# Performance work log

Hardware: AMD Instinct MI355X
Metric: run time of the kernel (lower is better)

The kernel has to match this reference:

```python
import jax, jax.numpy as jnp
import numpy as np

B, S, DM, H, DF = 2, 2048, 1024, 16, 4096
HD = DM // H
EPS = 1e-6
NEG = -1e9


def setup_inputs() -> dict:
    key = jax.random.key(0)
    ks = jax.random.split(key, 16)
    sc = 1.0 / np.sqrt(DM)
    scf = 1.0 / np.sqrt(DF)
    return {
        "x": jax.random.normal(ks[0], (B, S, DM), jnp.float32),
        "src_mask": jax.random.randint(ks[1], (B, 1, 1, S), 0, 2, jnp.int32),
        "Wq": jax.random.normal(ks[2], (DM, DM), jnp.float32) * sc,
        "bq": jnp.zeros((DM,), jnp.float32),
        "Wk": jax.random.normal(ks[3], (DM, DM), jnp.float32) * sc,
        "bk": jnp.zeros((DM,), jnp.float32),
        "Wv": jax.random.normal(ks[4], (DM, DM), jnp.float32) * sc,
        "bv": jnp.zeros((DM,), jnp.float32),
        "Wo": jax.random.normal(ks[5], (DM, DM), jnp.float32) * sc,
        "bo": jnp.zeros((DM,), jnp.float32),
        "W1": jax.random.normal(ks[6], (DM, DF), jnp.float32) * sc,
        "b1": jnp.zeros((DF,), jnp.float32),
        "W2": jax.random.normal(ks[7], (DF, DM), jnp.float32) * scf,
        "b2": jnp.zeros((DM,), jnp.float32),
        "alpha1": jnp.ones((1,), jnp.float32),
        "beta1": jnp.ones((1,), jnp.float32),
        "alpha2": jnp.ones((1,), jnp.float32),
        "beta2": jnp.ones((1,), jnp.float32),
    }


def layer_norm(x, alpha, beta):
    # torch: mean + unbiased std (ddof=1), scalar alpha/beta, eps added to std
    mean = jnp.mean(x, axis=-1, keepdims=True)
    std = jnp.std(x, axis=-1, keepdims=True, ddof=1)
    return alpha * (x - mean) / (std + EPS) + beta


def mha(x, mask, Wq, bq, Wk, bk, Wv, bv, Wo, bo):
    def split(t):  # [B,S,DM] -> [B,H,S,HD]
        return t.reshape(B, S, H, HD).transpose(0, 2, 1, 3)
    q = split(x @ Wq + bq)
    k = split(x @ Wk + bk)
    v = split(x @ Wv + bv)
    scores = jnp.einsum("bhqd,bhkd->bhqk", q, k) / np.sqrt(HD)
    scores = jnp.where(mask == 0, NEG, scores)
    probs = jax.nn.softmax(scores, axis=-1)  # dropout in eval mode = identity
    out = jnp.einsum("bhqk,bhkd->bhqd", probs, v)
    out = out.transpose(0, 2, 1, 3).reshape(B, S, DM)
    return out @ Wo + bo


def reference(x, src_mask, Wq, bq, Wk, bk, Wv, bv, Wo, bo, W1, b1, W2, b2,
              alpha1, beta1, alpha2, beta2):
    # pre-norm residual: x + attn(norm(x)); dropout disabled (eval)
    n1 = layer_norm(x, alpha1, beta1)
    h = x + mha(n1, src_mask, Wq, bq, Wk, bk, Wv, bv, Wo, bo)
    n2 = layer_norm(h, alpha2, beta2)
    ff = jax.nn.relu(n2 @ W1 + b1) @ W2 + b2
    return h + ff
```

## Files before the change

kernel.cpp:

```cpp
#include <hip/hip_runtime.h>
#include <hip/hip_bf16.h>

#define SEQ   2048
#define BATCH 2
#define DMODEL 1024
#define DFF   4096
#define NHEAD 16
#define HDIM  64
#define NTOK  (BATCH*SEQ)

typedef short s8v __attribute__((ext_vector_type(8)));
typedef float f4v __attribute__((ext_vector_type(4)));

__device__ __forceinline__ float b2f(unsigned short u) {
    union { unsigned int i; float f; } v; v.i = ((unsigned int)u) << 16; return v.f;
}
__device__ __forceinline__ unsigned short f2b(float f) {
    union { unsigned int i; float f; } v; v.f = f;
    unsigned int r = v.i + 0x7FFFu + ((v.i >> 16) & 1u);
    return (unsigned short)(r >> 16);
}
__device__ __forceinline__ ushort2 cvt_pk(float a, float b) {
    __hip_bfloat162 h = __float22bfloat162_rn(float2{ a, b });
    return *(ushort2*)&h;
}

__device__ __forceinline__ f4v mfma_bf16(s8v a, s8v b, f4v c) {
    return __builtin_amdgcn_mfma_f32_16x16x32_bf16(a, b, c, 0, 0, 0);
}

__device__ __forceinline__ void gload_lds16(const void* g, void* l) {
    __builtin_amdgcn_global_load_lds(
        (const __attribute__((address_space(1))) unsigned int*)g,
        (__attribute__((address_space(3))) unsigned int*)l, 16, 0, 0);
}

template<int N> __device__ __forceinline__ void wait_vmcnt() {
    if constexpr (N == 8)      asm volatile("s_waitcnt vmcnt(8)" ::: "memory");
    else if constexpr (N == 6) asm volatile("s_waitcnt vmcnt(6)" ::: "memory");
    else if constexpr (N == 4) asm volatile("s_waitcnt vmcnt(4)" ::: "memory");
    else if constexpr (N == 2) asm volatile("s_waitcnt vmcnt(2)" ::: "memory");
    else                       asm volatile("s_waitcnt vmcnt(0)" ::: "memory");
}

__device__ __forceinline__ void tp_tile(const float* __restrict__ src,
                                        unsigned short* __restrict__ dst,
                                        int R, int C, int br, int bc, int t,
                                        unsigned short* tl) {
    for (int i = 0; i < 16; i++) {
        int idx = t + 256 * i;
        int r = idx >> 6, c = idx & 63;
        tl[r * 65 + c] = f2b(src[(size_t)(br * 64 + r) * C + bc * 64 + c]);
    }
    __syncthreads();
    for (int i = 0; i < 16; i++) {
        int idx = t + 256 * i;
        int r2 = idx >> 6, c2 = idx & 63;
        dst[(size_t)(bc * 64 + r2) * R + br * 64 + c2] = tl[c2 * 65 + r2];
    }
}

__global__ __launch_bounds__(256) void prep_weights(const float* __restrict__ Wq,
                                                    const float* __restrict__ Wk,
                                                    const float* __restrict__ Wv,
                                                    const float* __restrict__ Wo,
                                                    const float* __restrict__ W1,
                                                    const float* __restrict__ W2,
                                                    const float* __restrict__ bq,
                                                    const float* __restrict__ bk,
                                                    const float* __restrict__ bv,
                                                    const float* __restrict__ x,
                                                    const float* __restrict__ a1,
                                                    const float* __restrict__ be1,
                                                    unsigned short* __restrict__ Wqkv_t,
                                                    unsigned short* __restrict__ Wo_t,
                                                    unsigned short* __restrict__ W1_t,
                                                    unsigned short* __restrict__ W2_t,
                                                    float* __restrict__ bqkv,
                                                    unsigned short* __restrict__ n1) {
    __shared__ unsigned short tl[64 * 65];
    __shared__ float red[8];
    const int t = threadIdx.x;
    const int bx = blockIdx.x, by = blockIdx.y, z = blockIdx.z;
    if (z < 4) {
        const float* src = (z == 0) ? Wq : (z == 1) ? Wk : (z == 2) ? Wv : Wo;
        unsigned short* dst = (z == 3) ? Wo_t : Wqkv_t + (size_t)z * 1024 * 1024;
        tp_tile(src, dst, 1024, 1024, bx, by, t, tl);
    } else if (z == 4) {
        for (int i = 0; i < 4; i++) {
            tp_tile(W1, W1_t, 1024, 4096, bx, by + 16 * i, t, tl);
            __syncthreads();
        }
    } else if (z == 5) {
        if (bx == 0 && by == 0) {
            for (int i = 0; i < 12; i++) {
                int idx = t + 256 * i;
                if (idx < 1024) bqkv[idx] = bq[idx];
                else if (idx < 2048) bqkv[idx] = bk[idx - 1024];
                else if (idx < 3072) bqkv[idx] = bv[idx - 2048];
            }
        }
        for (int i = 0; i < 4; i++) {
            tp_tile(W2, W2_t, 4096, 1024, bx + 16 * i, by, t, tl);
            __syncthreads();
        }
    } else {
        const int row = (z - 6) * 256 + by * 16 + bx;
        const float* xr = x + (size_t)row * DMODEL;
        float4 u = ((const float4*)xr)[t];
        float v[4] = { u.x, u.y, u.z, u.w };
        float s = v[0] + v[1] + v[2] + v[3];
        float sq = v[0]*v[0] + v[1]*v[1] + v[2]*v[2] + v[3]*v[3];
        for (int off = 32; off; off >>= 1) { s += __shfl_xor(s, off); sq += __shfl_xor(sq, off); }
        int wave = t >> 6, lane = t & 63;
        if (!lane) { red[wave] = s; red[4 + wave] = sq; }
        __syncthreads();
        s = red[0] + red[1] + red[2] + red[3];
        sq = red[4] + red[5] + red[6] + red[7];
        float mean = s * (1.f / DMODEL);
        float var = (sq - (float)DMODEL * mean * mean) * (1.f / (DMODEL - 1));
        var = var < 0.f ? 0.f : var;
        float inv = a1[0] / (sqrtf(var) + 1e-6f);
        float bt = be1[0];
        uint2 ou;
        unsigned short r0 = f2b((v[0] - mean) * inv + bt);
        unsigned short r1 = f2b((v[1] - mean) * inv + bt);
        unsigned short r2 = f2b((v[2] - mean) * inv + bt);
        unsigned short r3 = f2b((v[3] - mean) * inv + bt);
        ou.x = (unsigned int)r0 | ((unsigned int)r1 << 16);
        ou.y = (unsigned int)r2 | ((unsigned int)r3 << 16);
        ((uint2*)(n1 + (size_t)row * DMODEL))[t] = ou;
    }
}

__global__ __launch_bounds__(256) void mask_scan(const int* __restrict__ msk,
                                                 int* __restrict__ idx,
                                                 float* __restrict__ maskc2,
                                                 int* __restrict__ ntiles) {
    const int b = blockIdx.x, t = threadIdx.x;
    const int base = b * SEQ;
    __shared__ int wsum[4];
    int k[8]; int cnt = 0;
    for (int j = 0; j < 8; j++) {
        k[j] = (msk[base + t * 8 + j] != 0) ? 1 : 0;
        cnt += k[j];
    }
    const int lane = t & 63, wv = t >> 6;
    int pre = cnt;
    for (int off = 1; off < 64; off <<= 1) {
        int n = __shfl_up(pre, off);
        if (lane >= off) pre += n;
    }
    if (lane == 63) wsum[wv] = pre;
    __syncthreads();
    const int Nb = wsum[0] + wsum[1] + wsum[2] + wsum[3];
    int woff = 0;
    for (int w = 0; w < wv; w++) woff += wsum[w];
    const int excl = woff + pre - cnt;
    for (int j = 0; j < 8; j++) {
        int g = t * 8 + j;
        idx[base + g] = 0;
        maskc2[base + g] = (g < Nb) ? 0.f : -1e9f;
    }
    __syncthreads();
    int pos = excl;
    for (int j = 0; j < 8; j++) {
        if (k[j]) { idx[base + pos] = t * 8 + j; pos++; }
    }
    if (t == 0) ntiles[b] = (Nb + 63) >> 6;
}

__global__ __launch_bounds__(256) void pack_kv(const unsigned short* __restrict__ Kb,
                                               const unsigned short* __restrict__ Vb,
                                               const int* __restrict__ idx,
                                               const int* __restrict__ ntiles,
                                               unsigned short* __restrict__ Kc,
                                               unsigned short* __restrict__ Vc) {
    __shared__ unsigned short tl[64 * 65];
    const int t = threadIdx.x;
    const int kt = blockIdx.x, h = blockIdx.y, b = blockIdx.z;
    if (kt >= ntiles[b]) return;
    const int* idxb = idx + b * SEQ + kt * 64;
    const unsigned short* srcK = Kb + (size_t)b * SEQ * 1024 + h * HDIM;
    unsigned short* dstK = Kc + ((size_t)((b * NHEAD + h) * 32 + kt)) * 4096;
    for (int i = 0; i < 2; i++) {
        int ci = t + 256 * i;
        int r = ci >> 3, cp = ci & 7;
        int cl = cp ^ (r & 7);
        int row = idxb[r];
        *(uint4*)&dstK[ci * 8] = *(const uint4*)&srcK[(size_t)row * 1024 + cl * 8];
    }
    const unsigned short* srcV = Vb + (size_t)b * SEQ * 1024 + h * HDIM;
    for (int i = 0; i < 16; i++) {
        int idx2 = t + 256 * i;
        int r = idx2 >> 6, c = idx2 & 63;
        int row = idxb[r];
        tl[r * 65 + c] = srcV[(size_t)row * 1024 + c];
    }
    __syncthreads();
    unsigned short* dstV = Vc + ((size_t)((b * NHEAD + h) * 32 + kt)) * 4096;
    for (int i = 0; i < 2; i++) {
        int ci = t + 256 * i;
        int r = ci >> 3, cp = ci & 7;
        int cl = cp ^ (r & 7);
        ushort4 e0, e1;
        e0.x = tl[(cl * 8 + 0) * 65 + r]; e0.y = tl[(cl * 8 + 1) * 65 + r];
        e0.z = tl[(cl * 8 + 2) * 65 + r]; e0.w = tl[(cl * 8 + 3) * 65 + r];
        e1.x = tl[(cl * 8 + 4) * 65 + r]; e1.y = tl[(cl * 8 + 5) * 65 + r];
        e1.z = tl[(cl * 8 + 6) * 65 + r]; e1.w = tl[(cl * 8 + 7) * 65 + r];
        *(ushort4*)&dstV[ci * 8]     = e0;
        *(ushort4*)&dstV[ci * 8 + 4] = e1;
    }
}

__global__ __launch_bounds__(256) void ln_kernel(const float* __restrict__ x,
                                                 const float* __restrict__ al,
                                                 const float* __restrict__ be,
                                                 unsigned short* __restrict__ o) {
    const int row = blockIdx.x;
    const float* xr = x + (size_t)row * DMODEL;
    float4 u = ((const float4*)xr)[threadIdx.x];
    float v[4] = { u.x, u.y, u.z, u.w };
    float s = v[0] + v[1] + v[2] + v[3];
    float sq = v[0]*v[0] + v[1]*v[1] + v[2]*v[2] + v[3]*v[3];
    for (int off = 32; off; off >>= 1) { s += __shfl_xor(s, off); sq += __shfl_xor(sq, off); }
    __shared__ float red[8];
    int wave = threadIdx.x >> 6, lane = threadIdx.x & 63;
    if (!lane) { red[wave] = s; red[4 + wave] = sq; }
    __syncthreads();
    s = red[0] + red[1] + red[2] + red[3];
    sq = red[4] + red[5] + red[6] + red[7];
    float mean = s * (1.f / DMODEL);
    float var = (sq - (float)DMODEL * mean * mean) * (1.f / (DMODEL - 1));
    var = var < 0.f ? 0.f : var;
    float inv = al[0] / (sqrtf(var) + 1e-6f);
    float bt = be[0];
    uint2 ou;
    unsigned short r0 = f2b((v[0] - mean) * inv + bt);
    unsigned short r1 = f2b((v[1] - mean) * inv + bt);
    unsigned short r2 = f2b((v[2] - mean) * inv + bt);
    unsigned short r3 = f2b((v[3] - mean) * inv + bt);
    ou.x = (unsigned int)r0 | ((unsigned int)r1 << 16);
    ou.y = (unsigned int)r2 | ((unsigned int)r3 << 16);
    ((uint2*)(o + (size_t)row * DMODEL))[threadIdx.x] = ou;
}


template<int SPAN, int NL>
__device__ __forceinline__ void stage_half(const unsigned short* __restrict__ mat,
                                           int base, int K, int k0, int q,
                                           unsigned short* sdst, int t) {
#pragma unroll
    for (int i = 0; i < NL; i++) {
        int ci = i * 512 + t;
        int rl = ci >> 3;
        int c  = (ci & 7) ^ (rl & 7);
        int gr = (rl / SPAN) * (2 * SPAN) + q * SPAN + (rl % SPAN);
        gload_lds16(mat + (size_t)(base + gr) * K + k0 + c * 8, sdst + (size_t)ci * 8);
    }
}

__device__ __forceinline__ const s8v* afrag(const unsigned short* sA, int mi, int s,
                                            int wm, int l16, int quad) {
    int q = mi >> 2;
    int rl = wm * 64 + (mi & 3) * 16 + l16;
    return (const s8v*)&sA[q * 8192 + rl * 64 + (((s * 4 + quad) ^ (l16 & 7)) * 8)];
}
template<int BN>
__device__ __forceinline__ const s8v* bfrag(const unsigned short* sB, int ni, int s,
                                            int wn, int l16, int quad) {
    constexpr int NQB = BN / 128;
    int q = ni / NQB;
    int rl = wn * (BN / 8) + (ni % NQB) * 16 + l16;
    return (const s8v*)&sB[q * (BN * 32) + rl * 64 + (((s * 4 + quad) ^ (l16 & 7)) * 8)];
}

template<int BN>
__device__ __forceinline__ void half_8ph(const unsigned short* __restrict__ A,
                                         const unsigned short* __restrict__ Bt,
                                         int m0, int n0, int K, int kT1, int kT2, bool doT2,
                                         const unsigned short* sAr, const unsigned short* sBr,
                                         unsigned short* sA_this, unsigned short* sB_this,
                                         unsigned short* sA_oth,
                                         int wm, int wn, int l16, int quad, int t,
                                         f4v acc[8][BN / 64]) {
    constexpr int NFC = BN / 64, NQB = NFC / 2;
    constexpr int BSPAN = BN / 8, BNL = BN / 128, BHALF = BN * 32;
    s8v a[4][2], b[NFC][2];
#pragma unroll
    for (int m2 = 0; m2 < 4; m2++) {
        a[m2][0] = *afrag(sAr, m2, 0, wm, l16, quad);
        a[m2][1] = *afrag(sAr, m2, 1, wm, l16, quad);
    }
#pragma unroll
    for (int nb = 0; nb < NQB; nb++) {
        b[nb][0] = *bfrag<BN>(sBr, nb, 0, wn, l16, quad);
        b[nb][1] = *bfrag<BN>(sBr, nb, 1, wn, l16, quad);
    }
    stage_half<64, 2>(A, m0, K, kT1, 1, sA_oth + 8192, t);
    __builtin_amdgcn_s_barrier();
    asm volatile("s_waitcnt lgkmcnt(0)" ::: "memory");
    __builtin_amdgcn_s_setprio(1);
#pragma unroll
    for (int m2 = 0; m2 < 4; m2++)
#pragma unroll
        for (int nb = 0; nb < NQB; nb++) {
            acc[m2][nb] = mfma_bf16(a[m2][0], b[nb][0], acc[m2][nb]);
            acc[m2][nb] = mfma_bf16(a[m2][1], b[nb][1], acc[m2][nb]);
        }
    __builtin_amdgcn_s_setprio(0);
    __builtin_amdgcn_s_barrier();
#pragma unroll
    for (int nb = 0; nb < NQB; nb++) {
        b[NQB + nb][0] = *bfrag<BN>(sBr, NQB + nb, 0, wn, l16, quad);
        b[NQB + nb][1] = *bfrag<BN>(sBr, NQB + nb, 1, wn, l16, quad);
    }
    if (doT2) stage_half<64, 2>(A, m0, K, kT2, 0, sA_this, t);
    __builtin_amdgcn_s_barrier();
    asm volatile("s_waitcnt lgkmcnt(0)" ::: "memory");
    __builtin_amdgcn_s_setprio(1);
#pragma unroll
    for (int m2 = 0; m2 < 4; m2++)
#pragma unroll
        for (int nb = 0; nb < NQB; nb++) {
            acc[m2][NQB + nb] = mfma_bf16(a[m2][0], b[NQB + nb][0], acc[m2][NQB + nb]);
            acc[m2][NQB + nb] = mfma_bf16(a[m2][1], b[NQB + nb][1], acc[m2][NQB + nb]);
        }
    __builtin_amdgcn_s_setprio(0);
    __builtin_amdgcn_s_barrier();
#pragma unroll
    for (int m2 = 0; m2 < 4; m2++) {
        a[m2][0] = *afrag(sAr, 4 + m2, 0, wm, l16, quad);
        a[m2][1] = *afrag(sAr, 4 + m2, 1, wm, l16, quad);
    }
    if (doT2) stage_half<BSPAN, BNL>(Bt, n0, K, kT2, 0, sB_this, t);
    __builtin_amdgcn_s_barrier();
    asm volatile("s_waitcnt lgkmcnt(0)" ::: "memory");
    __builtin_amdgcn_s_setprio(1);
#pragma unroll
    for (int m2 = 0; m2 < 4; m2++)
#pragma unroll
        for (int nb = 0; nb < NQB; nb++) {
            acc[4 + m2][nb] = mfma_bf16(a[m2][0], b[nb][0], acc[4 + m2][nb]);
            acc[4 + m2][nb] = mfma_bf16(a[m2][1], b[nb][1], acc[4 + m2][nb]);
        }
    __builtin_amdgcn_s_setprio(0);
    __builtin_amdgcn_s_barrier();
    if (doT2) {
        stage_half<BSPAN, BNL>(Bt, n0, K, kT2, 1, sB_this + BHALF, t);
        if constexpr (BN == 256) wait_vmcnt<6>(); else wait_vmcnt<4>();
    } else {
        wait_vmcnt<0>();
    }
    __builtin_amdgcn_s_barrier();
    __builtin_amdgcn_s_setprio(1);
#pragma unroll
    for (int m2 = 0; m2 < 4; m2++)
#pragma unroll
        for (int nb = 0; nb < NQB; nb++) {
            acc[4 + m2][NQB + nb] = mfma_bf16(a[m2][0], b[NQB + nb][0], acc[4 + m2][NQB + nb]);
            acc[4 + m2][NQB + nb] = mfma_bf16(a[m2][1], b[NQB + nb][1], acc[4 + m2][NQB + nb]);
        }
    __builtin_amdgcn_s_setprio(0);
    __builtin_amdgcn_s_barrier();
}

template<int BN>
__device__ __forceinline__ void comp_full(const unsigned short* sA, const unsigned short* sB,
                                          int wm, int wn, int l16, int quad,
                                          f4v acc[8][BN / 64]) {
    constexpr int NFC = BN / 64;
    s8v b[NFC][2];
#pragma unroll
    for (int ni = 0; ni < NFC; ni++) {
        b[ni][0] = *bfrag<BN>(sB, ni, 0, wn, l16, quad);
        b[ni][1] = *bfrag<BN>(sB, ni, 1, wn, l16, quad);
    }
#pragma unroll
    for (int mi = 0; mi < 8; mi++) {
        s8v a0 = *afrag(sA, mi, 0, wm, l16, quad);
        s8v a1 = *afrag(sA, mi, 1, wm, l16, quad);
#pragma unroll
        for (int ni = 0; ni < NFC; ni++) {
            acc[mi][ni] = mfma_bf16(a0, b[ni][0], acc[mi][ni]);
            acc[mi][ni] = mfma_bf16(a1, b[ni][1], acc[mi][ni]);
        }
    }
}

template<bool RELU, bool RES, typename CT, bool SPLIT3, int BN>
__global__ __launch_bounds__(512, 2) void gemm256(const unsigned short* __restrict__ A,
                                                  const unsigned short* __restrict__ Bt,
                                                  const float* __restrict__ bias,
                                                  const float* __restrict__ res,
                                                  CT* __restrict__ C,
                                                  float* __restrict__ pbuf,
                                                  int M, int N, int K, int KS) {
    constexpr int NFC = BN / 64;
    constexpr int BHALF = BN * 32;
    __shared__ __align__(16) unsigned short smA[2][256 * 64];
    __shared__ __align__(16) unsigned short smB[2][BN * 64];
    const int t = threadIdx.x;
    const int wave = t >> 6, lane = t & 63;
    const int quad = lane >> 4, l16 = lane & 15;
    const int wm = wave >> 2, wn = wave & 3;
    const int m0 = blockIdx.x * 256, n0 = blockIdx.y * BN;
    const int z = blockIdx.z;
    const int kbeg = z * KS;
    const int nt = KS >> 6;

    f4v acc[8][NFC] = {};

    stage_half<64, 2>(A, m0, K, kbeg, 0, smA[0], t);
    stage_half<64, 2>(A, m0, K, kbeg, 1, smA[0] + 8192, t);
    stage_half<BN / 8, BN / 128>(Bt, n0, K, kbeg, 0, smB[0], t);
    stage_half<BN / 8, BN / 128>(Bt, n0, K, kbeg, 1, smB[0] + BHALF, t);
    stage_half<64, 2>(A, m0, K, kbeg + 64, 0, smA[1], t);
    stage_half<BN / 8, BN / 128>(Bt, n0, K, kbeg + 64, 0, smB[1], t);
    stage_half<BN / 8, BN / 128>(Bt, n0, K, kbeg + 64, 1, smB[1] + BHALF, t);
    if constexpr (BN == 256) wait_vmcnt<6>(); else wait_vmcnt<4>();
    __builtin_amdgcn_s_barrier();

    for (int i = 0; i < nt / 2 - 1; ++i) {
        const int kb = kbeg + 2 * i * 64;
        half_8ph<BN>(A, Bt, m0, n0, K, kb + 64, kb + 128, true,
                     smA[0], smB[0], smA[0], smB[0], smA[1],
                     wm, wn, l16, quad, t, acc);
        half_8ph<BN>(A, Bt, m0, n0, K, kb + 128, kb + 192, true,
                     smA[1], smB[1], smA[1], smB[1], smA[0],
                     wm, wn, l16, quad, t, acc);
    }
    half_8ph<BN>(A, Bt, m0, n0, K, kbeg + (nt - 1) * 64, 0, false,
                 smA[0], smB[0], smA[0], smB[0], smA[1],
                 wm, wn, l16, quad, t, acc);
    __builtin_amdgcn_s_setprio(1);
    comp_full<BN>(smA[1], smB[1], wm, wn, l16, quad, acc);
    __builtin_amdgcn_s_setprio(0);

#pragma unroll
    for (int mi = 0; mi < 8; mi++) {
#pragma unroll
        for (int ni = 0; ni < NFC; ni++) {
            const int col = n0 + wn * (NFC * 16) + ni * 16 + l16;
            const int row0 = m0 + wm * 128 + mi * 16 + quad * 4;
            if (z == 0) {
                const float bv = bias[col];
#pragma unroll
                for (int r = 0; r < 4; r++) {
                    float v = acc[mi][ni][r] + bv;
                    if (RELU) v = v > 0.f ? v : 0.f;
                    if (RES) v += res[(size_t)(row0 + r) * N + col];
                    size_t cidx;
                    if constexpr (SPLIT3)
                        cidx = (size_t)(col >> 10) * ((size_t)NTOK * 1024)
                             + (size_t)(row0 + r) * 1024 + (col & 1023);
                    else
                        cidx = (size_t)(row0 + r) * N + col;
                    if constexpr (sizeof(CT) == 2)
                        C[cidx] = f2b(v);
                    else
                        C[cidx] = v;
                }
            } else {
#pragma unroll
                for (int r = 0; r < 4; r++)
                    pbuf[(size_t)(z - 1) * M * N + (size_t)(row0 + r) * N + col]
                        = acc[mi][ni][r];
            }
        }
    }
}

__global__ __launch_bounds__(256) void add_pbuf(float* __restrict__ out,
                                                const float* __restrict__ pbuf) {
    const int i0 = (blockIdx.x * 256 + threadIdx.x) * 8;
    float4 a0 = *(const float4*)&out[i0];
    float4 a1 = *(const float4*)&out[i0 + 4];
    float4 p0 = *(const float4*)&pbuf[i0];
    float4 p1 = *(const float4*)&pbuf[i0 + 4];
    a0.x += p0.x; a0.y += p0.y; a0.z += p0.z; a0.w += p0.w;
    a1.x += p1.x; a1.y += p1.y; a1.z += p1.z; a1.w += p1.w;
    *(float4*)&out[i0]     = a0;
    *(float4*)&out[i0 + 4] = a1;
}

#define EXPC 0.18033688f
__device__ __forceinline__ void attn_tile(const unsigned short* __restrict__ smKb,
                                          const unsigned short* __restrict__ smVb,
                                          const float* __restrict__ smM, int k0,
                                          unsigned short* __restrict__ smPw,
                                          s8v qf0, s8v qf1, int quad, int l16,
                                          float& l_s, f4v* oacc) {
    const int l7 = l16 & 7;
    f4v s[4];
#pragma unroll
    for (int kt4 = 0; kt4 < 4; kt4++) {
        int r = kt4 * 16 + l16;
        s8v kf0 = *(const s8v*)&smKb[r * 64 + ((quad ^ l7) * 8)];
        s8v kf1 = *(const s8v*)&smKb[r * 64 + (((quad + 4) ^ l7) * 8)];
        f4v z = {};
        z = mfma_bf16(kf0, qf0, z);
        z = mfma_bf16(kf1, qf1, z);
        s[kt4] = z;
    }
#pragma unroll
    for (int kt4 = 0; kt4 < 4; kt4++) {
        float4 mf = *(const float4*)&smM[k0 + kt4 * 16 + quad * 4];
        s[kt4][0] = s[kt4][0] * EXPC + mf.x;
        s[kt4][1] = s[kt4][1] * EXPC + mf.y;
        s[kt4][2] = s[kt4][2] * EXPC + mf.z;
        s[kt4][3] = s[kt4][3] * EXPC + mf.w;
    }
#pragma unroll
    for (int kt4 = 0; kt4 < 4; kt4++)
#pragma unroll
        for (int r = 0; r < 4; r++) {
            float p = __builtin_amdgcn_exp2f(s[kt4][r]);
            s[kt4][r] = p;
            l_s += p;
        }
#pragma unroll
    for (int kt4 = 0; kt4 < 4; kt4++) {
        ushort2 p01 = cvt_pk(s[kt4][0], s[kt4][1]);
        ushort2 p23 = cvt_pk(s[kt4][2], s[kt4][3]);
        ushort4 pk;
        pk.x = p01.x; pk.y = p01.y; pk.z = p23.x; pk.w = p23.y;
        int c = kt4 * 2 + (quad >> 1);
        *(ushort4*)&smPw[l16 * 64 + ((c ^ l7) * 8 + (quad & 1) * 4)] = pk;
    }
    s8v pf0 = *(const s8v*)&smPw[l16 * 64 + ((quad ^ l7) * 8)];
    s8v pf1 = *(const s8v*)&smPw[l16 * 64 + (((quad + 4) ^ l7) * 8)];
#pragma unroll
    for (int nt = 0; nt < 4; nt++) {
        int r = nt * 16 + l16;
        s8v v0 = *(const s8v*)&smVb[r * 64 + ((quad ^ l7) * 8)];
        s8v v1 = *(const s8v*)&smVb[r * 64 + (((quad + 4) ^ l7) * 8)];
        oacc[nt] = mfma_bf16(pf0, v0, oacc[nt]);
        oacc[nt] = mfma_bf16(pf1, v1, oacc[nt]);
    }
}

__global__ __launch_bounds__(512) void attn_kernel(const unsigned short* __restrict__ Qb,
                                                   const unsigned short* __restrict__ Kc,
                                                   const unsigned short* __restrict__ Vc,
                                                   const float* __restrict__ maskc2,
                                                   const int* __restrict__ ntiles,
                                                   unsigned short* __restrict__ out) {
    __shared__ __align__(16) unsigned short smK[2][4096];
    __shared__ __align__(16) unsigned short smV[2][4096];
    __shared__ __align__(16) unsigned short smP[8][1024];
    __shared__ __align__(16) float smM[SEQ];

    const int t = threadIdx.x;
    const int wave = t >> 6, lane = t & 63;
    const int quad = lane >> 4, l16 = lane & 15;
    const int qt = blockIdx.x, h = blockIdx.y, b = blockIdx.z;
    const int q0 = qt * 128 + wave * 16;
    const int nt = ntiles[b];
    const unsigned short* Kbh = Kc + ((size_t)(b * NHEAD + h)) * 32 * 4096;
    const unsigned short* Vbh = Vc + ((size_t)(b * NHEAD + h)) * 32 * 4096;
    unsigned short* smPw = &smP[wave][0];

    const unsigned short* Qp = Qb + ((size_t)b * SEQ + q0 + l16) * 1024 + h * HDIM + quad * 8;
    s8v qf0 = *(const s8v*)(Qp);
    s8v qf1 = *(const s8v*)(Qp + 32);

    gload_lds16(maskc2 + (size_t)b * SEQ + t * 4, (float*)smM + t * 4);
    gload_lds16(Kbh + t * 8,        smK[0] + t * 8);
    gload_lds16(Vbh + t * 8,        smV[0] + t * 8);
    gload_lds16(Kbh + 4096 + t * 8, smK[1] + t * 8);
    gload_lds16(Vbh + 4096 + t * 8, smV[1] + t * 8);
    wait_vmcnt<2>();
    __builtin_amdgcn_s_barrier();

    float l_s = 0.f;
    f4v oacc[4] = {};

    for (int it = 0; it < nt; ++it) {
        const int cb = it & 1;
        __builtin_amdgcn_s_setprio(1);
        attn_tile(smK[cb], smV[cb], smM, it * 64, smPw, qf0, qf1, quad, l16, l_s, oacc);
        __builtin_amdgcn_s_setprio(0);
        if (it + 2 < nt) {
            asm volatile("s_waitcnt lgkmcnt(0)" ::: "memory");
            __builtin_amdgcn_s_barrier();
            gload_lds16(Kbh + (size_t)(it + 2) * 4096 + t * 8, smK[cb] + t * 8);
            gload_lds16(Vbh + (size_t)(it + 2) * 4096 + t * 8, smV[cb] + t * 8);
            wait_vmcnt<2>();
            __builtin_amdgcn_s_barrier();
        } else if (it + 1 < nt) {
            asm volatile("s_waitcnt lgkmcnt(0)" ::: "memory");
            __builtin_amdgcn_s_barrier();
            wait_vmcnt<0>();
            __builtin_amdgcn_s_barrier();
        }
    }

    l_s += __shfl_xor(l_s, 16);
    l_s += __shfl_xor(l_s, 32);
    float lrr[4];
    for (int r = 0; r < 4; r++) lrr[r] = __shfl(l_s, quad * 4 + r);
    for (int nt2 = 0; nt2 < 4; nt2++)
        for (int r = 0; r < 4; r++) {
            int row = q0 + quad * 4 + r;
            int col = h * HDIM + nt2 * 16 + l16;
            out[((size_t)b * SEQ + row) * DMODEL + col] = f2b(oacc[nt2][r] / lrr[r]);
        }
}

extern "C" void kernel_launch(void* const* d_in, const int* in_sizes, int n_in,
                              void* d_out, int out_size, void* d_ws, size_t ws_size,
                              hipStream_t stream) {
    const float* x   = (const float*)d_in[0];
    const int*   msk = (const int*)d_in[1];
    const float* Wq  = (const float*)d_in[2];
    const float* bq  = (const float*)d_in[3];
    const float* Wk  = (const float*)d_in[4];
    const float* bk  = (const float*)d_in[5];
    const float* Wv  = (const float*)d_in[6];
    const float* bv  = (const float*)d_in[7];
    const float* Wo  = (const float*)d_in[8];
    const float* bo  = (const float*)d_in[9];
    const float* W1  = (const float*)d_in[10];
    const float* b1  = (const float*)d_in[11];
    const float* W2  = (const float*)d_in[12];
    const float* b2  = (const float*)d_in[13];
    const float* a1  = (const float*)d_in[14];
    const float* be1 = (const float*)d_in[15];
    const float* a2  = (const float*)d_in[16];
    const float* be2 = (const float*)d_in[17];
    float* outf = (float*)d_out;

    char* ws = (char*)d_ws;
    const size_t MB = 1024 * 1024;
    unsigned short* W2_t   = (unsigned short*)(ws);
    unsigned short* W1_t   = (unsigned short*)(ws + 8 * MB);
    float*          Pbuf   = (float*)(ws + 8 * MB);
    unsigned short* Wqkv_t = (unsigned short*)(ws + 16 * MB);
    float*          bqkv   = (float*)(ws + 22 * MB);
    unsigned short* Kc     = (unsigned short*)(ws + 16 * MB);
    unsigned short* n2     = (unsigned short*)(ws + 16 * MB);
    unsigned short* Wo_t   = (unsigned short*)(ws + 24 * MB);
    unsigned short* Qb     = (unsigned short*)(ws + 26 * MB);
    unsigned short* Kb     = (unsigned short*)(ws + 34 * MB);
    unsigned short* Vb     = (unsigned short*)(ws + 42 * MB);
    float*          Pbuf2  = (float*)(ws + 34 * MB);
    unsigned short* ff1    = (unsigned short*)(ws + 26 * MB);
    unsigned short* attnO  = (unsigned short*)(ws + 50 * MB);
    unsigned short* n1     = (unsigned short*)d_out;
    unsigned short* Vc     = (unsigned short*)d_out;
    float*          hbuf   = (float*)d_out;
    float*          maskc2 = (float*)((char*)d_out + 8 * MB);
    int*            idxc   = (int*)((char*)d_out + 8 * MB + 16 * 1024);
    int*            ntl    = (int*)((char*)d_out + 8 * MB + 32 * 1024);

    mask_scan<<<dim3(BATCH), 256, 0, stream>>>(msk, idxc, maskc2, ntl);
    prep_weights<<<dim3(16, 16, 22), 256, 0, stream>>>(
        Wq, Wk, Wv, Wo, W1, W2, bq, bk, bv, x, a1, be1,
        Wqkv_t, Wo_t, W1_t, W2_t, bqkv, n1);

    gemm256<false, false, unsigned short, true, 256><<<dim3(16, 12, 1), 512, 0, stream>>>(
        n1, Wqkv_t, bqkv, nullptr, Qb, nullptr, NTOK, 3072, 1024, 1024);
    pack_kv<<<dim3(32, 16, 2), 256, 0, stream>>>(Kb, Vb, idxc, ntl, Kc, Vc);
    attn_kernel<<<dim3(16, 16, 2), 512, 0, stream>>>(Qb, Kc, Vc, maskc2, ntl, attnO);
    gemm256<false, true, float, false, 128><<<dim3(16, 8, 2), 512, 0, stream>>>(
        attnO, Wo_t, bo, x, hbuf, Pbuf2, NTOK, 1024, 1024, 512);
    add_pbuf<<<dim3(2048), 256, 0, stream>>>(hbuf, Pbuf2);
    ln_kernel<<<NTOK, 256, 0, stream>>>(hbuf, a2, be2, n2);
    gemm256<true, false, unsigned short, false, 256><<<dim3(16, 16, 1), 512, 0, stream>>>(
        n2, W1_t, b1, nullptr, ff1, nullptr, NTOK, DFF, 1024, 1024);
    gemm256<false, true, float, false, 128><<<dim3(16, 8, 2), 512, 0, stream>>>(
        ff1, W2_t, b2, hbuf, outf, Pbuf, NTOK, 1024, 4096, 2048);
    add_pbuf<<<dim3(2048), 256, 0, stream>>>(outf, Pbuf);
}
```

Baseline: 343.9 us.

## Add two-phase pipelined K-loop for BN=128 GEMM and fuse split-K add into LayerNorm

For the BN=128 split-K GEMMs (Wo and W2 projections), the unrolled-by-two 8-phase loop is replaced with a per-tile two-phase schedule. It loads both B fragments once, runs the two M halves with interleaved global staging, and alternates the double buffers each iteration. Separately, the split-K partial-sum addition for the attention output is folded into the second LayerNorm kernel, which removes one launch and one full read and write of the hidden buffer. The new pipeline uses different wait counts and staging order, so it risks stalls or hazards if the vmcnt accounting is off.

```diff
diff --git a/kernel.cpp b/kernel.cpp
--- a/kernel.cpp
+++ b/kernel.cpp
@@ -213,13 +213,18 @@
     }
 }
 
-__global__ __launch_bounds__(256) void ln_kernel(const float* __restrict__ x,
-                                                 const float* __restrict__ al,
-                                                 const float* __restrict__ be,
-                                                 unsigned short* __restrict__ o) {
+__global__ __launch_bounds__(256) void ln_add(float* __restrict__ hb,
+                                              const float* __restrict__ pbuf,
+                                              const float* __restrict__ al,
+                                              const float* __restrict__ be,
+                                              unsigned short* __restrict__ o) {
     const int row = blockIdx.x;
-    const float* xr = x + (size_t)row * DMODEL;
-    float4 u = ((const float4*)xr)[threadIdx.x];
+    float* hr = hb + (size_t)row * DMODEL;
+    const float* pr = pbuf + (size_t)row * DMODEL;
+    float4 u = ((const float4*)hr)[threadIdx.x];
+    float4 p = ((const float4*)pr)[threadIdx.x];
+    u.x += p.x; u.y += p.y; u.z += p.z; u.w += p.w;
+    ((float4*)hr)[threadIdx.x] = u;
     float v[4] = { u.x, u.y, u.z, u.w };
     float s = v[0] + v[1] + v[2] + v[3];
     float sq = v[0]*v[0] + v[1]*v[1] + v[2]*v[2] + v[3]*v[3];
@@ -348,7 +353,7 @@
     __builtin_amdgcn_s_barrier();
     if (doT2) {
         stage_half<BSPAN, BNL>(Bt, n0, K, kT2, 1, sB_this + BHALF, t);
-        if constexpr (BN == 256) wait_vmcnt<6>(); else wait_vmcnt<4>();
+        wait_vmcnt<6>();
     } else {
         wait_vmcnt<0>();
     }
@@ -360,6 +365,67 @@
         for (int nb = 0; nb < NQB; nb++) {
             acc[4 + m2][NQB + nb] = mfma_bf16(a[m2][0], b[NQB + nb][0], acc[4 + m2][NQB + nb]);
             acc[4 + m2][NQB + nb] = mfma_bf16(a[m2][1], b[NQB + nb][1], acc[4 + m2][NQB + nb]);
+        }
+    __builtin_amdgcn_s_setprio(0);
+    __builtin_amdgcn_s_barrier();
+}
+
+__device__ __forceinline__ void tile_2ph(const unsigned short* __restrict__ A,
+                                         const unsigned short* __restrict__ Bt,
+                                         int m0, int n0, int K, int kT1, int kT2,
+                                         bool doT1, bool doT2,
+                                         const unsigned short* sAr, const unsigned short* sBr,
+                                         unsigned short* sA_this, unsigned short* sB_this,
+                                         unsigned short* sA_oth,
+                                         int wm, int wn, int l16, int quad, int t,
+                                         f4v acc[8][2]) {
+    s8v a[4][2], b[2][2];
+#pragma unroll
+    for (int m2 = 0; m2 < 4; m2++) {
+        a[m2][0] = *afrag(sAr, m2, 0, wm, l16, quad);
+        a[m2][1] = *afrag(sAr, m2, 1, wm, l16, quad);
+    }
+#pragma unroll
+    for (int ni = 0; ni < 2; ni++) {
+        b[ni][0] = *bfrag<128>(sBr, ni, 0, wn, l16, quad);
+        b[ni][1] = *bfrag<128>(sBr, ni, 1, wn, l16, quad);
+    }
+    if (doT1) stage_half<64, 2>(A, m0, K, kT1, 1, sA_oth + 8192, t);
+    __builtin_amdgcn_s_barrier();
+    asm volatile("s_waitcnt lgkmcnt(0)" ::: "memory");
+    __builtin_amdgcn_s_setprio(1);
+#pragma unroll
+    for (int m2 = 0; m2 < 4; m2++)
+#pragma unroll
+        for (int ni = 0; ni < 2; ni++) {
+            acc[m2][ni] = mfma_bf16(a[m2][0], b[ni][0], acc[m2][ni]);
+            acc[m2][ni] = mfma_bf16(a[m2][1], b[ni][1], acc[m2][ni]);
+        }
+    __builtin_amdgcn_s_setprio(0);
+    __builtin_amdgcn_s_barrier();
+    s8v a2[4][2];
+#pragma unroll
+    for (int m2 = 0; m2 < 4; m2++) {
+        a2[m2][0] = *afrag(sAr, 4 + m2, 0, wm, l16, quad);
+        a2[m2][1] = *afrag(sAr, 4 + m2, 1, wm, l16, quad);
+    }
+    if (doT2) {
+        stage_half<64, 2>(A, m0, K, kT2, 0, sA_this, t);
+        stage_half<16, 1>(Bt, n0, K, kT2, 0, sB_this, t);
+        stage_half<16, 1>(Bt, n0, K, kT2, 1, sB_this + 128 * 32, t);
+        wait_vmcnt<6>();
+    } else if (doT1) {
+        wait_vmcnt<0>();
+    }
+    __builtin_amdgcn_s_barrier();
+    asm volatile("s_waitcnt lgkmcnt(0)" ::: "memory");
+    __builtin_amdgcn_s_setprio(1);
+#pragma unroll
+    for (int m2 = 0; m2 < 4; m2++)
+#pragma unroll
+        for (int ni = 0; ni < 2; ni++) {
+            acc[4 + m2][ni] = mfma_bf16(a2[m2][0], b[ni][0], acc[4 + m2][ni]);
+            acc[4 + m2][ni] = mfma_bf16(a2[m2][1], b[ni][1], acc[4 + m2][ni]);
         }
     __builtin_amdgcn_s_setprio(0);
     __builtin_amdgcn_s_barrier();
@@ -411,31 +477,51 @@
 
     f4v acc[8][NFC] = {};
 
-    stage_half<64, 2>(A, m0, K, kbeg, 0, smA[0], t);
-    stage_half<64, 2>(A, m0, K, kbeg, 1, smA[0] + 8192, t);
-    stage_half<BN / 8, BN / 128>(Bt, n0, K, kbeg, 0, smB[0], t);
-    stage_half<BN / 8, BN / 128>(Bt, n0, K, kbeg, 1, smB[0] + BHALF, t);
-    stage_half<64, 2>(A, m0, K, kbeg + 64, 0, smA[1], t);
-    stage_half<BN / 8, BN / 128>(Bt, n0, K, kbeg + 64, 0, smB[1], t);
-    stage_half<BN / 8, BN / 128>(Bt, n0, K, kbeg + 64, 1, smB[1] + BHALF, t);
-    if constexpr (BN == 256) wait_vmcnt<6>(); else wait_vmcnt<4>();
-    __builtin_amdgcn_s_barrier();
-
-    for (int i = 0; i < nt / 2 - 1; ++i) {
-        const int kb = kbeg + 2 * i * 64;
-        half_8ph<BN>(A, Bt, m0, n0, K, kb + 64, kb + 128, true,
+    if constexpr (BN == 256) {
+        stage_half<64, 2>(A, m0, K, kbeg, 0, smA[0], t);
+        stage_half<64, 2>(A, m0, K, kbeg, 1, smA[0] + 8192, t);
+        stage_half<BN / 8, BN / 128>(Bt, n0, K, kbeg, 0, smB[0], t);
+        stage_half<BN / 8, BN / 128>(Bt, n0, K, kbeg, 1, smB[0] + BHALF, t);
+        stage_half<64, 2>(A, m0, K, kbeg + 64, 0, smA[1], t);
+        stage_half<BN / 8, BN / 128>(Bt, n0, K, kbeg + 64, 0, smB[1], t);
+        stage_half<BN / 8, BN / 128>(Bt, n0, K, kbeg + 64, 1, smB[1] + BHALF, t);
+        wait_vmcnt<6>();
+        __builtin_amdgcn_s_barrier();
+
+        for (int i = 0; i < nt / 2 - 1; ++i) {
+            const int kb = kbeg + 2 * i * 64;
+            half_8ph<BN>(A, Bt, m0, n0, K, kb + 64, kb + 128, true,
+                         smA[0], smB[0], smA[0], smB[0], smA[1],
+                         wm, wn, l16, quad, t, acc);
+            half_8ph<BN>(A, Bt, m0, n0, K, kb + 128, kb + 192, true,
+                         smA[1], smB[1], smA[1], smB[1], smA[0],
+                         wm, wn, l16, quad, t, acc);
+        }
+        half_8ph<BN>(A, Bt, m0, n0, K, kbeg + (nt - 1) * 64, 0, false,
                      smA[0], smB[0], smA[0], smB[0], smA[1],
                      wm, wn, l16, quad, t, acc);
-        half_8ph<BN>(A, Bt, m0, n0, K, kb + 128, kb + 192, true,
-                     smA[1], smB[1], smA[1], smB[1], smA[0],
+        __builtin_amdgcn_s_setprio(1);
+        comp_full<BN>(smA[1], smB[1], wm, wn, l16, quad, acc);
+        __builtin_amdgcn_s_setprio(0);
+    } else {
+        stage_half<64, 2>(A, m0, K, kbeg, 0, smA[0], t);
+        stage_half<64, 2>(A, m0, K, kbeg, 1, smA[0] + 8192, t);
+        stage_half<16, 1>(Bt, n0, K, kbeg, 0, smB[0], t);
+        stage_half<16, 1>(Bt, n0, K, kbeg, 1, smB[0] + BHALF, t);
+        stage_half<64, 2>(A, m0, K, kbeg + 64, 0, smA[1], t);
+        stage_half<16, 1>(Bt, n0, K, kbeg + 64, 0, smB[1], t);
+        stage_half<16, 1>(Bt, n0, K, kbeg + 64, 1, smB[1] + BHALF, t);
+        wait_vmcnt<4>();
+        __builtin_amdgcn_s_barrier();
+
+        for (int it = 0; it < nt; ++it) {
+            const int cb = it & 1;
+            tile_2ph(A, Bt, m0, n0, K, kbeg + (it + 1) * 64, kbeg + (it + 2) * 64,
+                     it + 1 < nt, it + 2 < nt,
+                     smA[cb], smB[cb], smA[cb], smB[cb], smA[cb ^ 1],
                      wm, wn, l16, quad, t, acc);
-    }
-    half_8ph<BN>(A, Bt, m0, n0, K, kbeg + (nt - 1) * 64, 0, false,
-                 smA[0], smB[0], smA[0], smB[0], smA[1],
-                 wm, wn, l16, quad, t, acc);
-    __builtin_amdgcn_s_setprio(1);
-    comp_full<BN>(smA[1], smB[1], wm, wn, l16, quad, acc);
-    __builtin_amdgcn_s_setprio(0);
+        }
+    }
 
 #pragma unroll
     for (int mi = 0; mi < 8; mi++) {
@@ -665,8 +751,7 @@
     attn_kernel<<<dim3(16, 16, 2), 512, 0, stream>>>(Qb, Kc, Vc, maskc2, ntl, attnO);
     gemm256<false, true, float, false, 128><<<dim3(16, 8, 2), 512, 0, stream>>>(
         attnO, Wo_t, bo, x, hbuf, Pbuf2, NTOK, 1024, 1024, 512);
-    add_pbuf<<<dim3(2048), 256, 0, stream>>>(hbuf, Pbuf2);
-    ln_kernel<<<NTOK, 256, 0, stream>>>(hbuf, a2, be2, n2);
+    ln_add<<<NTOK, 256, 0, stream>>>(hbuf, Pbuf2, a2, be2, n2);
     gemm256<true, false, unsigned short, false, 256><<<dim3(16, 16, 1), 512, 0, stream>>>(
         n2, W1_t, b1, nullptr, ff1, nullptr, NTOK, DFF, 1024, 1024);
     gemm256<false, true, float, false, 128><<<dim3(16, 8, 2), 512, 0, stream>>>(
```

Result: faster. 333.6 us (-3.0%).

## Replace split-K partial buffers with atomic accumulation and fuse residual add into LayerNorm

Applied to the files above, without the earlier changes.

The two split-K output GEMMs (Wo and W2) now use 256-wide N tiles with a 4-way K split and accumulate straight into the destination with float atomicAdd. This removes the partial-sum buffers and the separate add_pbuf kernels. The attention-projection residual is folded into a new ln_add kernel, which sums x with the atomically accumulated projection, writes h, and normalizes in one pass. That kernel needs a memset of the accumulator beforehand. The weight-transpose prep also switches to float4 loads and ushort4 stores. The tradeoff is atomic contention and nondeterministic summation order.

```diff
diff --git a/kernel.cpp b/kernel.cpp
--- a/kernel.cpp
+++ b/kernel.cpp
@@ -47,16 +47,25 @@
                                         unsigned short* __restrict__ dst,
                                         int R, int C, int br, int bc, int t,
                                         unsigned short* tl) {
-    for (int i = 0; i < 16; i++) {
-        int idx = t + 256 * i;
-        int r = idx >> 6, c = idx & 63;
-        tl[r * 65 + c] = f2b(src[(size_t)(br * 64 + r) * C + bc * 64 + c]);
+    for (int i = 0; i < 4; i++) {
+        int lin = i * 1024 + t * 4;
+        int r = lin >> 6, c = lin & 63;
+        float4 u = *(const float4*)&src[(size_t)(br * 64 + r) * C + bc * 64 + c];
+        tl[r * 65 + c + 0] = f2b(u.x);
+        tl[r * 65 + c + 1] = f2b(u.y);
+        tl[r * 65 + c + 2] = f2b(u.z);
+        tl[r * 65 + c + 3] = f2b(u.w);
     }
     __syncthreads();
-    for (int i = 0; i < 16; i++) {
-        int idx = t + 256 * i;
-        int r2 = idx >> 6, c2 = idx & 63;
-        dst[(size_t)(bc * 64 + r2) * R + br * 64 + c2] = tl[c2 * 65 + r2];
+    for (int i = 0; i < 4; i++) {
+        int lin = i * 1024 + t * 4;
+        int r2 = lin >> 6, c2 = lin & 63;
+        ushort4 o;
+        o.x = tl[(c2 + 0) * 65 + r2];
+        o.y = tl[(c2 + 1) * 65 + r2];
+        o.z = tl[(c2 + 2) * 65 + r2];
+        o.w = tl[(c2 + 3) * 65 + r2];
+        *(ushort4*)&dst[(size_t)(bc * 64 + r2) * R + br * 64 + c2] = o;
     }
 }
 
@@ -213,13 +222,17 @@
     }
 }
 
-__global__ __launch_bounds__(256) void ln_kernel(const float* __restrict__ x,
-                                                 const float* __restrict__ al,
-                                                 const float* __restrict__ be,
-                                                 unsigned short* __restrict__ o) {
+__global__ __launch_bounds__(256) void ln_add(const float* __restrict__ x,
+                                              const float* __restrict__ ws,
+                                              const float* __restrict__ al,
+                                              const float* __restrict__ be,
+                                              float* __restrict__ hb,
+                                              unsigned short* __restrict__ o) {
     const int row = blockIdx.x;
-    const float* xr = x + (size_t)row * DMODEL;
-    float4 u = ((const float4*)xr)[threadIdx.x];
+    float4 u = ((const float4*)(x + (size_t)row * DMODEL))[threadIdx.x];
+    float4 p = ((const float4*)(ws + (size_t)row * DMODEL))[threadIdx.x];
+    u.x += p.x; u.y += p.y; u.z += p.z; u.w += p.w;
+    ((float4*)(hb + (size_t)row * DMODEL))[threadIdx.x] = u;
     float v[4] = { u.x, u.y, u.z, u.w };
     float s = v[0] + v[1] + v[2] + v[3];
     float sq = v[0]*v[0] + v[1]*v[1] + v[2]*v[2] + v[3]*v[3];
@@ -266,16 +279,13 @@
     int rl = wm * 64 + (mi & 3) * 16 + l16;
     return (const s8v*)&sA[q * 8192 + rl * 64 + (((s * 4 + quad) ^ (l16 & 7)) * 8)];
 }
-template<int BN>
 __device__ __forceinline__ const s8v* bfrag(const unsigned short* sB, int ni, int s,
                                             int wn, int l16, int quad) {
-    constexpr int NQB = BN / 128;
-    int q = ni / NQB;
-    int rl = wn * (BN / 8) + (ni % NQB) * 16 + l16;
-    return (const s8v*)&sB[q * (BN * 32) + rl * 64 + (((s * 4 + quad) ^ (l16 & 7)) * 8)];
-}
-
-template<int BN>
+    int q = ni >> 1;
+    int rl = wn * 32 + (ni & 1) * 16 + l16;
+    return (const s8v*)&sB[q * 8192 + rl * 64 + (((s * 4 + quad) ^ (l16 & 7)) * 8)];
+}
+
 __device__ __forceinline__ void half_8ph(const unsigned short* __restrict__ A,
                                          const unsigned short* __restrict__ Bt,
                                          int m0, int n0, int K, int kT1, int kT2, bool doT2,
@@ -283,19 +293,17 @@
                                          unsigned short* sA_this, unsigned short* sB_this,
                                          unsigned short* sA_oth,
                                          int wm, int wn, int l16, int quad, int t,
-                                         f4v acc[8][BN / 64]) {
-    constexpr int NFC = BN / 64, NQB = NFC / 2;
-    constexpr int BSPAN = BN / 8, BNL = BN / 128, BHALF = BN * 32;
-    s8v a[4][2], b[NFC][2];
+                                         f4v acc[8][4]) {
+    s8v a[4][2], b[4][2];
 #pragma unroll
     for (int m2 = 0; m2 < 4; m2++) {
         a[m2][0] = *afrag(sAr, m2, 0, wm, l16, quad);
         a[m2][1] = *afrag(sAr, m2, 1, wm, l16, quad);
     }
 #pragma unroll
-    for (int nb = 0; nb < NQB; nb++) {
-        b[nb][0] = *bfrag<BN>(sBr, nb, 0, wn, l16, quad);
-        b[nb][1] = *bfrag<BN>(sBr, nb, 1, wn, l16, quad);
+    for (int nb = 0; nb < 2; nb++) {
+        b[nb][0] = *bfrag(sBr, nb, 0, wn, l16, quad);
+        b[nb][1] = *bfrag(sBr, nb, 1, wn, l16, quad);
     }
     stage_half<64, 2>(A, m0, K, kT1, 1, sA_oth + 8192, t);
     __builtin_amdgcn_s_barrier();
@@ -304,16 +312,16 @@
 #pragma unroll
     for (int m2 = 0; m2 < 4; m2++)
 #pragma unroll
-        for (int nb = 0; nb < NQB; nb++) {
+        for (int nb = 0; nb < 2; nb++) {
             acc[m2][nb] = mfma_bf16(a[m2][0], b[nb][0], acc[m2][nb]);
             acc[m2][nb] = mfma_bf16(a[m2][1], b[nb][1], acc[m2][nb]);
         }
     __builtin_amdgcn_s_setprio(0);
     __builtin_amdgcn_s_barrier();
 #pragma unroll
-    for (int nb = 0; nb < NQB; nb++) {
-        b[NQB + nb][0] = *bfrag<BN>(sBr, NQB + nb, 0, wn, l16, quad);
-        b[NQB + nb][1] = *bfrag<BN>(sBr, NQB + nb, 1, wn, l16, quad);
+    for (int nb = 0; nb < 2; nb++) {
+        b[2 + nb][0] = *bfrag(sBr, 2 + nb, 0, wn, l16, quad);
+        b[2 + nb][1] = *bfrag(sBr, 2 + nb, 1, wn, l16, quad);
     }
     if (doT2) stage_half<64, 2>(A, m0, K, kT2, 0, sA_this, t);
     __builtin_amdgcn_s_barrier();
@@ -322,9 +330,9 @@
 #pragma unroll
     for (int m2 = 0; m2 < 4; m2++)
 #pragma unroll
-        for (int nb = 0; nb < NQB; nb++) {
-            acc[m2][NQB + nb] = mfma_bf16(a[m2][0], b[NQB + nb][0], acc[m2][NQB + nb]);
-            acc[m2][NQB + nb] = mfma_bf16(a[m2][1], b[NQB + nb][1], acc[m2][NQB + nb]);
+        for (int nb = 0; nb < 2; nb++) {
+            acc[m2][2 + nb] = mfma_bf16(a[m2][0], b[2 + nb][0], acc[m2][2 + nb]);
+            acc[m2][2 + nb] = mfma_bf16(a[m2][1], b[2 + nb][1], acc[m2][2 + nb]);
         }
     __builtin_amdgcn_s_setprio(0);
     __builtin_amdgcn_s_barrier();
@@ -333,22 +341,22 @@
         a[m2][0] = *afrag(sAr, 4 + m2, 0, wm, l16, quad);
         a[m2][1] = *afrag(sAr, 4 + m2, 1, wm, l16, quad);
     }
-    if (doT2) stage_half<BSPAN, BNL>(Bt, n0, K, kT2, 0, sB_this, t);
+    if (doT2) stage_half<32, 2>(Bt, n0, K, kT2, 0, sB_this, t);
     __builtin_amdgcn_s_barrier();
     asm volatile("s_waitcnt lgkmcnt(0)" ::: "memory");
     __builtin_amdgcn_s_setprio(1);
 #pragma unroll
     for (int m2 = 0; m2 < 4; m2++)
 #pragma unroll
-        for (int nb = 0; nb < NQB; nb++) {
+        for (int nb = 0; nb < 2; nb++) {
             acc[4 + m2][nb] = mfma_bf16(a[m2][0], b[nb][0], acc[4 + m2][nb]);
             acc[4 + m2][nb] = mfma_bf16(a[m2][1], b[nb][1], acc[4 + m2][nb]);
         }
     __builtin_amdgcn_s_setprio(0);
     __builtin_amdgcn_s_barrier();
     if (doT2) {
-        stage_half<BSPAN, BNL>(Bt, n0, K, kT2, 1, sB_this + BHALF, t);
-        if constexpr (BN == 256) wait_vmcnt<6>(); else wait_vmcnt<4>();
+        stage_half<32, 2>(Bt, n0, K, kT2, 1, sB_this + 8192, t);
+        wait_vmcnt<6>();
     } else {
         wait_vmcnt<0>();
     }
@@ -357,99 +365,94 @@
 #pragma unroll
     for (int m2 = 0; m2 < 4; m2++)
 #pragma unroll
-        for (int nb = 0; nb < NQB; nb++) {
-            acc[4 + m2][NQB + nb] = mfma_bf16(a[m2][0], b[NQB + nb][0], acc[4 + m2][NQB + nb]);
-            acc[4 + m2][NQB + nb] = mfma_bf16(a[m2][1], b[NQB + nb][1], acc[4 + m2][NQB + nb]);
+        for (int nb = 0; nb < 2; nb++) {
+            acc[4 + m2][2 + nb] = mfma_bf16(a[m2][0], b[2 + nb][0], acc[4 + m2][2 + nb]);
+            acc[4 + m2][2 + nb] = mfma_bf16(a[m2][1], b[2 + nb][1], acc[4 + m2][2 + nb]);
         }
     __builtin_amdgcn_s_setprio(0);
     __builtin_amdgcn_s_barrier();
 }
 
-template<int BN>
 __device__ __forceinline__ void comp_full(const unsigned short* sA, const unsigned short* sB,
                                           int wm, int wn, int l16, int quad,
-                                          f4v acc[8][BN / 64]) {
-    constexpr int NFC = BN / 64;
-    s8v b[NFC][2];
-#pragma unroll
-    for (int ni = 0; ni < NFC; ni++) {
-        b[ni][0] = *bfrag<BN>(sB, ni, 0, wn, l16, quad);
-        b[ni][1] = *bfrag<BN>(sB, ni, 1, wn, l16, quad);
+                                          f4v acc[8][4]) {
+    s8v b[4][2];
+#pragma unroll
+    for (int ni = 0; ni < 4; ni++) {
+        b[ni][0] = *bfrag(sB, ni, 0, wn, l16, quad);
+        b[ni][1] = *bfrag(sB, ni, 1, wn, l16, quad);
     }
 #pragma unroll
     for (int mi = 0; mi < 8; mi++) {
         s8v a0 = *afrag(sA, mi, 0, wm, l16, quad);
         s8v a1 = *afrag(sA, mi, 1, wm, l16, quad);
 #pragma unroll
-        for (int ni = 0; ni < NFC; ni++) {
+        for (int ni = 0; ni < 4; ni++) {
             acc[mi][ni] = mfma_bf16(a0, b[ni][0], acc[mi][ni]);
             acc[mi][ni] = mfma_bf16(a1, b[ni][1], acc[mi][ni]);
         }
     }
 }
 
-template<bool RELU, bool RES, typename CT, bool SPLIT3, int BN>
+template<bool RELU, typename CT, bool SPLIT3, bool ATOM>
 __global__ __launch_bounds__(512, 2) void gemm256(const unsigned short* __restrict__ A,
                                                   const unsigned short* __restrict__ Bt,
                                                   const float* __restrict__ bias,
-                                                  const float* __restrict__ res,
                                                   CT* __restrict__ C,
-                                                  float* __restrict__ pbuf,
                                                   int M, int N, int K, int KS) {
-    constexpr int NFC = BN / 64;
-    constexpr int BHALF = BN * 32;
     __shared__ __align__(16) unsigned short smA[2][256 * 64];
-    __shared__ __align__(16) unsigned short smB[2][BN * 64];
+    __shared__ __align__(16) unsigned short smB[2][256 * 64];
     const int t = threadIdx.x;
     const int wave = t >> 6, lane = t & 63;
     const int quad = lane >> 4, l16 = lane & 15;
     const int wm = wave >> 2, wn = wave & 3;
-    const int m0 = blockIdx.x * 256, n0 = blockIdx.y * BN;
+    const int m0 = blockIdx.x * 256, n0 = blockIdx.y * 256;
     const int z = blockIdx.z;
     const int kbeg = z * KS;
     const int nt = KS >> 6;
 
-    f4v acc[8][NFC] = {};
+    f4v acc[8][4] = {};
 
     stage_half<64, 2>(A, m0, K, kbeg, 0, smA[0], t);
     stage_half<64, 2>(A, m0, K, kbeg, 1, smA[0] + 8192, t);
-    stage_half<BN / 8, BN / 128>(Bt, n0, K, kbeg, 0, smB[0], t);
-    stage_half<BN / 8, BN / 128>(Bt, n0, K, kbeg, 1, smB[0] + BHALF, t);
+    stage_half<32, 2>(Bt, n0, K, kbeg, 0, smB[0], t);
+    stage_half<32, 2>(Bt, n0, K, kbeg, 1, smB[0] + 8192, t);
     stage_half<64, 2>(A, m0, K, kbeg + 64, 0, smA[1], t);
-    stage_half<BN / 8, BN / 128>(Bt, n0, K, kbeg + 64, 0, smB[1], t);
-    stage_half<BN / 8, BN / 128>(Bt, n0, K, kbeg + 64, 1, smB[1] + BHALF, t);
-    if constexpr (BN == 256) wait_vmcnt<6>(); else wait_vmcnt<4>();
+    stage_half<32, 2>(Bt, n0, K, kbeg + 64, 0, smB[1], t);
+    stage_half<32, 2>(Bt, n0, K, kbeg + 64, 1, smB[1] + 8192, t);
+    wait_vmcnt<6>();
     __builtin_amdgcn_s_barrier();
 
     for (int i = 0; i < nt / 2 - 1; ++i) {
         const int kb = kbeg + 2 * i * 64;
-        half_8ph<BN>(A, Bt, m0, n0, K, kb + 64, kb + 128, true,
-                     smA[0], smB[0], smA[0], smB[0], smA[1],
-                     wm, wn, l16, quad, t, acc);
-        half_8ph<BN>(A, Bt, m0, n0, K, kb + 128, kb + 192, true,
-                     smA[1], smB[1], smA[1], smB[1], smA[0],
-                     wm, wn, l16, quad, t, acc);
-    }
-    half_8ph<BN>(A, Bt, m0, n0, K, kbeg + (nt - 1) * 64, 0, false,
+        half_8ph(A, Bt, m0, n0, K, kb + 64, kb + 128, true,
                  smA[0], smB[0], smA[0], smB[0], smA[1],
                  wm, wn, l16, quad, t, acc);
+        half_8ph(A, Bt, m0, n0, K, kb + 128, kb + 192, true,
+                 smA[1], smB[1], smA[1], smB[1], smA[0],
+                 wm, wn, l16, quad, t, acc);
+    }
+    half_8ph(A, Bt, m0, n0, K, kbeg + (nt - 1) * 64, 0, false,
+             smA[0], smB[0], smA[0], smB[0], smA[1],
+             wm, wn, l16, quad, t, acc);
     __builtin_amdgcn_s_setprio(1);
-    comp_full<BN>(smA[1], smB[1], wm, wn, l16, quad, acc);
+    comp_full(smA[1], smB[1], wm, wn, l16, quad, acc);
     __builtin_amdgcn_s_setprio(0);
 
 #pragma unroll
     for (int mi = 0; mi < 8; mi++) {
 #pragma unroll
-        for (int ni = 0; ni < NFC; ni++) {
-            const int col = n0 + wn * (NFC * 16) + ni * 16 + l16;
+        for (int ni = 0; ni < 4; ni++) {
+            const int col = n0 + wn * 64 + ni * 16 + l16;
             const int row0 = m0 + wm * 128 + mi * 16 + quad * 4;
-            if (z == 0) {
-                const float bv = bias[col];
-#pragma unroll
-                for (int r = 0; r < 4; r++) {
-                    float v = acc[mi][ni][r] + bv;
-                    if (RELU) v = v > 0.f ? v : 0.f;
-                    if (RES) v += res[(size_t)(row0 + r) * N + col];
+            const float bv = (!ATOM || z == 0) ? bias[col] : 0.f;
+#pragma unroll
+            for (int r = 0; r < 4; r++) {
+                float v = acc[mi][ni][r] + bv;
+                if (RELU) v = v > 0.f ? v : 0.f;
+                if constexpr (ATOM) {
+                    atomicAdd((float*)&C[(size_t)(row0 + r) * N + col], v);
+                } else {
                     size_t cidx;
                     if constexpr (SPLIT3)
                         cidx = (size_t)(col >> 10) * ((size_t)NTOK * 1024)
@@ -461,27 +464,9 @@
                     else
                         C[cidx] = v;
                 }
-            } else {
-#pragma unroll
-                for (int r = 0; r < 4; r++)
-                    pbuf[(size_t)(z - 1) * M * N + (size_t)(row0 + r) * N + col]
-                        = acc[mi][ni][r];
             }
         }
     }
-}
-
-__global__ __launch_bounds__(256) void add_pbuf(float* __restrict__ out,
-                                                const float* __restrict__ pbuf) {
-    const int i0 = (blockIdx.x * 256 + threadIdx.x) * 8;
-    float4 a0 = *(const float4*)&out[i0];
-    float4 a1 = *(const float4*)&out[i0 + 4];
-    float4 p0 = *(const float4*)&pbuf[i0];
-    float4 p1 = *(const float4*)&pbuf[i0 + 4];
-    a0.x += p0.x; a0.y += p0.y; a0.z += p0.z; a0.w += p0.w;
-    a1.x += p1.x; a1.y += p1.y; a1.z += p1.z; a1.w += p1.w;
-    *(float4*)&out[i0]     = a0;
-    *(float4*)&out[i0 + 4] = a1;
 }
 
 #define EXPC 0.18033688f
@@ -635,7 +620,6 @@
     const size_t MB = 1024 * 1024;
     unsigned short* W2_t   = (unsigned short*)(ws);
     unsigned short* W1_t   = (unsigned short*)(ws + 8 * MB);
-    float*          Pbuf   = (float*)(ws + 8 * MB);
     unsigned short* Wqkv_t = (unsigned short*)(ws + 16 * MB);
     float*          bqkv   = (float*)(ws + 22 * MB);
     unsigned short* Kc     = (unsigned short*)(ws + 16 * MB);
@@ -644,7 +628,7 @@
     unsigned short* Qb     = (unsigned short*)(ws + 26 * MB);
     unsigned short* Kb     = (unsigned short*)(ws + 34 * MB);
     unsigned short* Vb     = (unsigned short*)(ws + 42 * MB);
-    float*          Pbuf2  = (float*)(ws + 34 * MB);
+    float*          wsum   = (float*)(ws + 34 * MB);
     unsigned short* ff1    = (unsigned short*)(ws + 26 * MB);
     unsigned short* attnO  = (unsigned short*)(ws + 50 * MB);
     unsigned short* n1     = (unsigned short*)d_out;
@@ -659,17 +643,16 @@
         Wq, Wk, Wv, Wo, W1, W2, bq, bk, bv, x, a1, be1,
         Wqkv_t, Wo_t, W1_t, W2_t, bqkv, n1);
 
-    gemm256<false, false, unsigned short, true, 256><<<dim3(16, 12, 1), 512, 0, stream>>>(
-        n1, Wqkv_t, bqkv, nullptr, Qb, nullptr, NTOK, 3072, 1024, 1024);
+    gemm256<false, unsigned short, true, false><<<dim3(16, 12, 1), 512, 0, stream>>>(
+        n1, Wqkv_t, bqkv, Qb, NTOK, 3072, 1024, 1024);
     pack_kv<<<dim3(32, 16, 2), 256, 0, stream>>>(Kb, Vb, idxc, ntl, Kc, Vc);
+    hipMemsetAsync(wsum, 0, (size_t)NTOK * DMODEL * sizeof(float), stream);
     attn_kernel<<<dim3(16, 16, 2), 512, 0, stream>>>(Qb, Kc, Vc, maskc2, ntl, attnO);
-    gemm256<false, true, float, false, 128><<<dim3(16, 8, 2), 512, 0, stream>>>(
-        attnO, Wo_t, bo, x, hbuf, Pbuf2, NTOK, 1024, 1024, 512);
-    add_pbuf<<<dim3(2048), 256, 0, stream>>>(hbuf, Pbuf2);
-    ln_kernel<<<NTOK, 256, 0, stream>>>(hbuf, a2, be2, n2);
-    gemm256<true, false, unsigned short, false, 256><<<dim3(16, 16, 1), 512, 0, stream>>>(
-        n2, W1_t, b1, nullptr, ff1, nullptr, NTOK, DFF, 1024, 1024);
-    gemm256<false, true, float, false, 128><<<dim3(16, 8, 2), 512, 0, stream>>>(
-        ff1, W2_t, b2, hbuf, outf, Pbuf, NTOK, 1024, 4096, 2048);
-    add_pbuf<<<dim3(2048), 256, 0, stream>>>(outf, Pbuf);
-}
+    gemm256<false, float, false, true><<<dim3(16, 4, 4), 512, 0, stream>>>(
+        attnO, Wo_t, bo, wsum, NTOK, 1024, 1024, 256);
+    ln_add<<<NTOK, 256, 0, stream>>>(x, wsum, a2, be2, hbuf, n2);
+    gemm256<true, unsigned short, false, false><<<dim3(16, 16, 1), 512, 0, stream>>>(
+        n2, W1_t, b1, ff1, NTOK, DFF, 1024, 1024);
+    gemm256<false, float, false, true><<<dim3(16, 4, 4), 512, 0, stream>>>(
+        ff1, W2_t, b2, outf, NTOK, 1024, 4096, 1024);
+}
```

After: 391.3 us. 13.8% more time.
